# Kernel tuning notes

Measured on AMD Instinct MI355X. Metric: run time of the kernel, lower is better.

## Reference

```python
import jax, jax.numpy as jnp
import numpy as np

B, L, D_IN, D_MODEL, N_LAYERS, D_STATE, D_OUT = 32, 1024, 3, 512, 4, 64, 10


def setup_inputs() -> dict:
    key = jax.random.key(0)
    ks = jax.random.split(key, 6)
    x = jax.random.normal(ks[0], (B, L, D_IN), jnp.float32)
    W_enc = jax.random.normal(ks[1], (D_IN, D_MODEL), jnp.float32) / np.sqrt(D_IN)
    # per-channel log timestep, standard S4 init range [1e-3, 1e-1]
    log_dt = jax.random.uniform(ks[2], (N_LAYERS, D_MODEL), jnp.float32,
                                minval=np.log(1e-3), maxval=np.log(1e-1))
    # S4D-real init: A_n = -(n + 1/2), stored as log of magnitude
    A_log = jnp.broadcast_to(
        jnp.log(0.5 + jnp.arange(D_STATE, dtype=jnp.float32)),
        (N_LAYERS, D_MODEL, D_STATE)) * jnp.ones((), jnp.float32)
    C = jax.random.normal(ks[3], (N_LAYERS, D_MODEL, D_STATE), jnp.float32) / np.sqrt(D_STATE)
    W_ff = jax.random.normal(ks[4], (N_LAYERS, D_MODEL, D_MODEL), jnp.float32) / np.sqrt(D_MODEL)
    W_dec = jax.random.normal(ks[5], (D_MODEL, D_OUT), jnp.float32) / np.sqrt(D_MODEL)
    return dict(x=x, W_enc=W_enc, log_dt=log_dt, A_log=A_log, C=C, W_ff=W_ff, W_dec=W_dec)


def _s4d(x, log_dt, A_log, C):
    """Diagonal real S4D layer (is_real=True, skip=False, identity activation).
    x: (B, L, H); log_dt: (H,); A_log, C: (H, N).
    """
    Lx = x.shape[1]
    dt = jnp.exp(log_dt)                         # (H,)
    A = -jnp.exp(A_log)                          # (H, N) real negative poles
    dtA = dt[:, None] * A                        # (H, N)
    Bbar = (jnp.exp(dtA) - 1.0) / A              # ZOH discretization with B = 1
    # Vandermonde kernel: K[h, l] = sum_n (C*Bbar)[h, n] * exp(dtA[h, n] * l)
    lrange = jnp.arange(Lx, dtype=x.dtype)
    K = jnp.einsum('hn,hnl->hl', C * Bbar, jnp.exp(dtA[:, :, None] * lrange))
    # causal depthwise convolution via FFT (linear conv, pad to 2L)
    n = 2 * Lx
    Kf = jnp.fft.rfft(K, n=n, axis=-1)           # (H, n//2+1)
    xf = jnp.fft.rfft(x, n=n, axis=1)            # (B, n//2+1, H)
    y = jnp.fft.irfft(xf * Kf.T[None], n=n, axis=1)[:, :Lx]
    return y


def reference(x, W_enc, log_dt, A_log, C, W_ff, W_dec):
    h = x @ W_enc                                # (B, L, d_model), bias=False
    for i in range(N_LAYERS):
        h = _s4d(h, log_dt[i], A_log[i], C[i])   # S4D layer
        # dropout is identity at inference; FF block: Linear(no bias) + ReLU
        h = jax.nn.relu(h @ W_ff[i])
    out = h @ W_dec                              # (B, L, d_output)
    return out[:, -1, :]                         # get_last=True -> (B, d_output)
```

## Files before the change

### kernel.cpp

```cpp
#include <hip/hip_runtime.h>
#include <math.h>

#define B_   32
#define L_   1024
#define BT_  (B_*L_)
#define DIN  3
#define H_   512
#define NL   4
#define NS   64
#define DOUT 10
#define CT   128
#define NC   (L_/CT)
#define BH   (B_*H_)

typedef __attribute__((ext_vector_type(8))) _Float16 f16x8;
typedef __attribute__((ext_vector_type(4))) float f32x4;

__device__ inline void gload16(const void* g, void* l) {
    __builtin_amdgcn_global_load_lds((const __attribute__((address_space(1))) void*)g,
                                     (__attribute__((address_space(3))) void*)l, 16, 0, 0);
}

#define PSW(row, col) ((row) * 64 + ((col) ^ (((row) & 7) << 3)))

#define RAW_BARRIER() do { \
    asm volatile("s_waitcnt lgkmcnt(0)" ::: "memory"); \
    __builtin_amdgcn_s_barrier(); \
    asm volatile("" ::: "memory"); } while (0)

__global__ __launch_bounds__(512, 4) void conv_fused(const float* __restrict__ x,
                                                     const float* __restrict__ Wenc,
                                                     const float* __restrict__ log_dt,
                                                     const float* __restrict__ A_log,
                                                     const float* __restrict__ Cmat,
                                                     const float* __restrict__ WffL,
                                                     _Float16* __restrict__ WTl,
                                                     const _Float16* __restrict__ XT,
                                                     _Float16* __restrict__ YT,
                                                     float* __restrict__ ylast,
                                                     int layer, int doY) {
    __shared__ __align__(16) _Float16 smem[32768];
    __shared__ float Kl4[4][128];
    __shared__ float Kl[128];
    __shared__ float dAs[64];
    __shared__ float wps[64];
    __shared__ float rTs[64];
    _Float16* Vl  = smem;
    _Float16* Xh0 = smem + 8192;
    _Float16* Pl  = smem + 16384;
    _Float16* X1r = smem + 24576;
    _Float16* S0l = smem + 24576;
    _Float16* Bp  = smem;

    int bid = blockIdx.x;
    int h = bid >> 1, mh = bid & 1;
    int tid = threadIdx.x;
    int w = tid >> 6, l = tid & 63;
    const int fr = l & 15, q = l >> 4;
    const int wm = w >> 1, wn = w & 1;
    const _Float16* Xh = XT + (size_t)h * BT_ + (size_t)mh * 16384;

    const int c = l & 7, rsub = l >> 3;
    float w0e = 0.f, w1e = 0.f, w2e = 0.f;
    if (layer == 0) { w0e = Wenc[h]; w1e = Wenc[H_ + h]; w2e = Wenc[2 * H_ + h]; }

    if (layer == 0) {
#pragma unroll
        for (int s = 0; s < 2; s++) {
            _Float16* dst = s ? X1r : Xh0;
#pragma unroll
            for (int ii = 0; ii < 2; ii++) {
                int t2 = w * 2 + ii;
                int rr = t2 * 8 + rsub;
                int srcc = c ^ (rr & 7);
                int bt = mh * 16384 + rr * 128 + s * 64 + srcc * 8;
                const float* xp = x + (size_t)bt * DIN;
                f16x8 o;
#pragma unroll
                for (int e = 0; e < 8; e++)
                    o[e] = (_Float16)fmaf(xp[e * 3], w0e,
                                     fmaf(xp[e * 3 + 1], w1e, xp[e * 3 + 2] * w2e));
                *(f16x8*)&dst[t2 * 512 + l * 8] = o;
            }
        }
    } else {
#pragma unroll
        for (int s = 0; s < 2; s++) {
            _Float16* dst = s ? X1r : Xh0;
#pragma unroll
            for (int ii = 0; ii < 2; ii++) {
                int t2 = w * 2 + ii;
                int rr = t2 * 8 + rsub;
                int srcc = c ^ (rr & 7);
                gload16(Xh + (size_t)rr * 128 + s * 64 + srcc * 8,
                        &dst[t2 * 512 + l * 8]);
            }
        }
    }

    if (tid < 64) {
        int n = tid;
        float dt  = expf(log_dt[layer * H_ + h]);
        float A   = -expf(A_log[((size_t)layer * H_ + h) * NS + n]);
        float dtA = dt * A;
        float r0  = expf(dtA);
        dAs[n] = dtA;
        wps[n] = Cmat[((size_t)layer * H_ + h) * NS + n] * ((r0 - 1.0f) / A);
        rTs[n] = expf(dtA * (float)CT);
    } else if (layer < 3 && tid < 96) {
        int g = bid * 32 + (tid - 64);
        int n = g >> 6, k8 = g & 63;
        const float* src = WffL + n;
        f16x8 o;
#pragma unroll
        for (int j = 0; j < 8; j++)
            o[j] = (_Float16)src[(size_t)(k8 * 8 + j) * H_];
        *(f16x8*)(WTl + (size_t)n * H_ + k8 * 8) = o;
    }
    RAW_BARRIER();

#pragma unroll
    for (int ii = 0; ii < 2; ii++) {
        int slot = tid + 512 * ii;
        int n = slot >> 4, cc = slot & 15;
        float da = dAs[n];
        int jb = cc * 8;
        float cur  = __expf(da * (float)(127 - jb));
        float rinv = __expf(-da);
        f16x8 vv;
#pragma unroll
        for (int e = 0; e < 8; e++) { vv[e] = (_Float16)cur; cur *= rinv; }
        *(f16x8*)&Vl[n * 128 + ((cc >> 3) * 8 + ((cc & 7) ^ (n & 7))) * 8] = vv;
    }
    if (doY) {
        int t = tid & 127, g = tid >> 7;
        float k = 0.f, d = (float)t;
        for (int n = g * 16; n < g * 16 + 16; n++) k += wps[n] * __expf(dAs[n] * d);
        Kl4[g][t] = k;
    }
    __syncthreads();

    if (doY && tid < 128)
        Kl[tid] = (Kl4[0][tid] + Kl4[1][tid]) + (Kl4[2][tid] + Kl4[3][tid]);

    f16x8 fA[2][2][2];
    f32x4 accP[2][2] = {};
#pragma unroll
    for (int i = 0; i < 2; i++)
#pragma unroll
        for (int kk = 0; kk < 2; kk++) {
            int row = wm * 32 + i * 16 + fr;
            int kc = kk * 4 + q;
            fA[i][0][kk] = *(const f16x8*)&Xh0[row * 64 + ((kc ^ (row & 7)) * 8)];
            fA[i][1][kk] = *(const f16x8*)&X1r[row * 64 + ((kc ^ (row & 7)) * 8)];
        }
#pragma unroll
    for (int s = 0; s < 2; s++)
#pragma unroll
        for (int kk = 0; kk < 2; kk++) {
            int kc = kk * 4 + q;
            f16x8 bv[2];
#pragma unroll
            for (int j = 0; j < 2; j++) {
                int n = wn * 32 + j * 16 + fr;
                bv[j] = *(const f16x8*)&Vl[n * 128 + s * 64 + ((kc ^ (n & 7)) * 8)];
            }
#pragma unroll
            for (int i = 0; i < 2; i++)
#pragma unroll
                for (int j = 0; j < 2; j++)
                    accP[i][j] = __builtin_amdgcn_mfma_f32_16x16x32_f16(
                        fA[i][s][kk], bv[j], accP[i][j], 0, 0, 0);
        }

#pragma unroll
    for (int i = 0; i < 2; i++)
#pragma unroll
        for (int j = 0; j < 2; j++)
#pragma unroll
            for (int tt = 0; tt < 4; tt++) {
                int row = wm * 32 + i * 16 + q * 4 + tt;
                int col = wn * 32 + j * 16 + fr;
                Pl[PSW(row, col)] = (_Float16)accP[i][j][tt];
            }
    __syncthreads();

#pragma unroll
    for (int ii = 0; ii < 2; ii++) {
        int slot = tid + 512 * ii;
        int bl = slot >> 6, n = slot & 63;
        float rTn = rTs[n];
        float E = 0.f;
        if (doY) {
#pragma unroll
            for (int cc = 0; cc < 8; cc++) {
                int row = bl * 8 + cc;
                S0l[row * 64 + (((n >> 3) ^ (row & 7)) * 8 + (n & 7))] = (_Float16)E;
                E = fmaf(rTn, E, (float)Pl[PSW(row, n)]);
            }
        } else {
#pragma unroll
            for (int cc = 0; cc < 8; cc++) {
                int row = bl * 8 + cc;
                E = fmaf(rTn, E, (float)Pl[PSW(row, n)]);
            }
            float wE = wps[n] * E;
            wE += __shfl_xor(wE, 32); wE += __shfl_xor(wE, 16);
            wE += __shfl_xor(wE, 8);  wE += __shfl_xor(wE, 4);
            wE += __shfl_xor(wE, 2);  wE += __shfl_xor(wE, 1);
            if (l == 0) ylast[(size_t)(mh * 16 + bl) * H_ + h] = wE;
        }
    }
    if (!doY) return;
    __syncthreads();

#pragma unroll
    for (int ii = 0; ii < 2; ii++) {
        int slot = tid + 512 * ii;
        int n = slot & 63, tc = slot >> 6;
        int t0 = tc * 8;
        float ratio = __expf(dAs[n]);
        float cur   = wps[n] * __expf(dAs[n] * (float)(t0 + 1));
#pragma unroll
        for (int e = 0; e < 8; e++) {
            Bp[(t0 + e) * 192 + (16 + ((n >> 3) ^ e)) * 8 + (n & 7)] = (_Float16)cur;
            cur *= ratio;
        }
    }
#pragma unroll
    for (int ii = 0; ii < 4; ii++) {
        int slot = tid + 512 * ii;
        int t = slot >> 4, cc = slot & 15;
        _Float16* bp = &Bp[t * 192 + ((cc >> 3) * 8 + ((cc & 7) ^ (t & 7))) * 8];
        int jb = cc * 8;
#pragma unroll
        for (int e = 0; e < 8; e++) {
            int j = jb + e;
            bp[e] = (j <= t) ? (_Float16)Kl[t - j] : (_Float16)0.f;
        }
    }
    __syncthreads();

    f32x4 acc[2][4] = {};
#pragma unroll
    for (int s = 0; s < 3; s++)
#pragma unroll
        for (int kk = 0; kk < 2; kk++) {
            int kc = kk * 4 + q;
            f16x8 av[2], bv[4];
#pragma unroll
            for (int i = 0; i < 2; i++) {
                int row = wm * 32 + i * 16 + fr;
                av[i] = (s < 2) ? fA[i][s][kk]
                                : *(const f16x8*)&S0l[row * 64 + ((kc ^ (row & 7)) * 8)];
            }
#pragma unroll
            for (int j = 0; j < 4; j++) {
                int tc = wn * 64 + j * 16 + fr;
                bv[j] = *(const f16x8*)&Bp[tc * 192 + (s * 8 + (kc ^ (tc & 7))) * 8];
            }
#pragma unroll
            for (int i = 0; i < 2; i++)
#pragma unroll
                for (int j = 0; j < 4; j++)
                    acc[i][j] = __builtin_amdgcn_mfma_f32_16x16x32_f16(av[i], bv[j], acc[i][j], 0, 0, 0);
        }

    __syncthreads();
#pragma unroll
    for (int i = 0; i < 2; i++)
#pragma unroll
        for (int j = 0; j < 4; j++)
#pragma unroll
            for (int tt = 0; tt < 4; tt++) {
                int row = wm * 32 + i * 16 + q * 4 + tt;
                int col = wn * 64 + j * 16 + fr;
                smem[row * 136 + col] = (_Float16)acc[i][j][tt];
            }
    __syncthreads();
    _Float16* Yp = YT + (size_t)h * BT_ + (size_t)mh * 16384;
#pragma unroll
    for (int k2 = 0; k2 < 4; k2++) {
        int ch = tid + 512 * k2;
        int r = ch >> 4, c8 = ch & 15;
        *(f16x8*)(Yp + (size_t)r * 128 + c8 * 8) = *(const f16x8*)&smem[r * 136 + c8 * 8];
    }
}

__global__ __launch_bounds__(256) void ffn_gemm_T(
    const _Float16* __restrict__ WT,
    const _Float16* __restrict__ YT,
    _Float16* __restrict__ OT)
{
    __shared__ __align__(16) _Float16 pool[20736];
    _Float16* As0 = pool;
    _Float16* Bs0 = pool + 12288;
    const int tid = threadIdx.x;
    const int l = tid & 63, w = tid >> 6;
    const int bt0 = blockIdx.x * 128;
    const int bn  = blockIdx.y * 128;
    const int srow = l >> 2, schunk = (l & 3) ^ ((l >> 3) & 3);
    const _Float16* ga0 = WT + (size_t)(bn + (w * 2 + 0) * 16 + srow) * H_ + schunk * 8;
    const _Float16* ga1 = WT + (size_t)(bn + (w * 2 + 1) * 16 + srow) * H_ + schunk * 8;
    const int btg = tid & 15, kp = tid >> 4;
    const _Float16* gb = YT + (size_t)(kp * 2) * BT_ + bt0 + btg * 8;

    f16x8 stB[2][2];
    f32x4 acc[4][4] = {};

    auto loadB = [&](int ks, int st) {
        stB[st][0] = *(const f16x8*)(gb + (size_t)(ks * 32) * BT_);
        stB[st][1] = *(const f16x8*)(gb + (size_t)(ks * 32 + 1) * BT_);
    };
    auto stageA = [&](int ks, int buf) {
        gload16(ga0 + ks * 32, As0 + buf * 4096 + (w * 2 + 0) * 512);
        gload16(ga1 + ks * 32, As0 + buf * 4096 + (w * 2 + 1) * 512);
    };
    auto writeB = [&](int st, int buf) {
        const int kpc = kp >> 2, kps = kp & 3;
#pragma unroll
        for (int e = 0; e < 8; e++) {
            int row = btg * 8 + e;
            int off = row * 32 + (row >> 3) * 8 + ((kpc ^ ((row >> 1) & 3)) * 8) + kps * 2;
            _Float16 lo = stB[st][0][e], hi = stB[st][1][e];
            unsigned v = (unsigned)__builtin_bit_cast(unsigned short, lo)
                       | ((unsigned)__builtin_bit_cast(unsigned short, hi) << 16);
            *(unsigned*)&Bs0[buf * 4224 + off] = v;
        }
    };

    loadB(0, 0);
    loadB(1, 1);
    __builtin_amdgcn_sched_barrier(0);
    stageA(0, 0);
    stageA(1, 1);
    writeB(0, 0);
    asm volatile("s_waitcnt vmcnt(2) lgkmcnt(0)" ::: "memory");
    __builtin_amdgcn_s_barrier();
    asm volatile("" ::: "memory");

    const int wm = w >> 1, wn = w & 1;
    const int fr = l & 15, q = l >> 4;
    const int axor = ((fr >> 1) & 3);
#pragma unroll
    for (int ks = 0; ks < 16; ks++) {
        const int a_cur = ks % 3;
        const int b_cur = ks & 1;
        if (ks + 2 < 16) {
            loadB(ks + 2, b_cur);
            __builtin_amdgcn_sched_barrier(0);
            stageA(ks + 2, (ks + 2) % 3);
        }
        f16x8 av[4], bv[4];
#pragma unroll
        for (int i = 0; i < 4; i++) {
            int row = wm * 64 + i * 16 + fr;
            av[i] = *(const f16x8*)&As0[a_cur * 4096 + row * 32 + ((q ^ axor) * 8)];
        }
#pragma unroll
        for (int j = 0; j < 4; j++) {
            int row = wn * 64 + j * 16 + fr;
            bv[j] = *(const f16x8*)&Bs0[b_cur * 4224 + row * 32 + (row >> 3) * 8
                                        + ((q ^ ((row >> 1) & 3)) * 8)];
        }
#pragma unroll
        for (int i = 0; i < 4; i++)
#pragma unroll
            for (int j = 0; j < 4; j++)
                acc[i][j] = __builtin_amdgcn_mfma_f32_16x16x32_f16(av[i], bv[j], acc[i][j], 0, 0, 0);
        if (ks + 1 < 16) {
            writeB((ks + 1) & 1, b_cur ^ 1);
            if (ks + 2 < 16)
                asm volatile("s_waitcnt vmcnt(4) lgkmcnt(0)" ::: "memory");
            else
                asm volatile("s_waitcnt vmcnt(0) lgkmcnt(0)" ::: "memory");
            __builtin_amdgcn_s_barrier();
            asm volatile("" ::: "memory");
        }
    }
    asm volatile("s_waitcnt lgkmcnt(0)" ::: "memory");
    __builtin_amdgcn_s_barrier();
    asm volatile("" ::: "memory");

#pragma unroll
    for (int half = 0; half < 2; half++) {
        if (half) __syncthreads();
        if (wm == half) {
#pragma unroll
            for (int i = 0; i < 4; i++)
#pragma unroll
                for (int j = 0; j < 4; j++)
#pragma unroll
                    for (int tt = 0; tt < 4; tt++) {
                        int r  = i * 16 + q * 4 + tt;
                        int cc = wn * 64 + j * 16 + fr;
                        pool[r * 136 + cc] = (_Float16)fmaxf(acc[i][j][tt], 0.f);
                    }
        }
        __syncthreads();
#pragma unroll
        for (int k2 = 0; k2 < 4; k2++) {
            int ch = tid + 256 * k2;
            int r = ch >> 4, c8 = ch & 15;
            *(f16x8*)(OT + (size_t)(bn + half * 64 + r) * BT_ + bt0 + c8 * 8) =
                *(const f16x8*)&pool[r * 136 + c8 * 8];
        }
    }
}

__global__ __launch_bounds__(512) void final_head(const float* __restrict__ ylast,
                                                  const float* __restrict__ Wff3,
                                                  const float* __restrict__ Wdec,
                                                  float* __restrict__ out) {
    int b = blockIdx.x;
    int t = threadIdx.x;
    __shared__ float yrow[H_];
    __shared__ float hrow[H_];
    yrow[t] = ylast[(size_t)b * H_ + t];
    __syncthreads();
    float acc = 0.f;
    for (int k = 0; k < H_; k++) acc = fmaf(yrow[k], Wff3[(size_t)k * H_ + t], acc);
    hrow[t] = fmaxf(acc, 0.f);
    __syncthreads();
    if (t < DOUT) {
        float o = 0.f;
        for (int k = 0; k < H_; k++) o = fmaf(hrow[k], Wdec[(size_t)k * DOUT + t], o);
        out[(size_t)b * DOUT + t] = o;
    }
}

extern "C" void kernel_launch(void* const* d_in, const int* in_sizes, int n_in,
                              void* d_out, int out_size, void* d_ws, size_t ws_size,
                              hipStream_t stream) {
    const float* x      = (const float*)d_in[0];
    const float* Wenc   = (const float*)d_in[1];
    const float* log_dt = (const float*)d_in[2];
    const float* A_log  = (const float*)d_in[3];
    const float* Cmat   = (const float*)d_in[4];
    const float* Wff    = (const float*)d_in[5];
    const float* Wdec   = (const float*)d_in[6];
    float* out = (float*)d_out;

    char* ws = (char*)d_ws;
    _Float16* bufA  = (_Float16*)(ws);
    _Float16* bufB  = (_Float16*)(ws + 33554432);
    _Float16* WT    = (_Float16*)(ws + 68681728);
    float*    ylast = (float*)(ws + 70254592);

    for (int l = 0; l < NL; l++) {
        if (l < NL - 1) {
            conv_fused<<<H_ * 2, 512, 0, stream>>>(x, Wenc, log_dt, A_log, Cmat,
                                                   Wff + (size_t)l * H_ * H_,
                                                   WT + (size_t)l * H_ * H_,
                                                   bufA, bufB, ylast, l, 1);
            ffn_gemm_T<<<dim3(BT_ / 128, H_ / 128), 256, 0, stream>>>(
                WT + (size_t)l * H_ * H_, bufB, bufA);
        } else {
            conv_fused<<<H_ * 2, 512, 0, stream>>>(x, Wenc, log_dt, A_log, Cmat,
                                                   Wff + (size_t)l * H_ * H_,
                                                   WT,
                                                   bufA, bufB, ylast, l, 0);
            final_head<<<B_, 512, 0, stream>>>(ylast, Wff + (size_t)l * H_ * H_, Wdec, out);
        }
    }
}
```

Baseline: 211.3 us.

## Widen FFN GEMM tile to 256 columns and parallelize final head

The FFN GEMM block grows from 256 to 512 threads, and each block now covers 256 batch-time columns instead of 128. The 128-row weight tile is shared across twice as many columns and each thread stages one A chunk instead of two, with the wait counts and LDS strides adjusted to match. The final head is split into 8 blocks per batch row: each computes a 64-column slice with split-K partial sums and atomically adds its decoder contribution into an output that conv layer 0 zeroes. The costs are more LDS per GEMM block, fewer GEMM blocks, and float atomics in the head, which make the summation order nondeterministic.

```diff
diff --git a/kernel.cpp b/kernel.cpp
--- a/kernel.cpp
+++ b/kernel.cpp
@@ -38,6 +38,7 @@
                                                      const _Float16* __restrict__ XT,
                                                      _Float16* __restrict__ YT,
                                                      float* __restrict__ ylast,
+                                                     float* __restrict__ outz,
                                                      int layer, int doY) {
     __shared__ __align__(16) _Float16 smem[32768];
     __shared__ float Kl4[4][128];
@@ -65,6 +66,7 @@
     if (layer == 0) { w0e = Wenc[h]; w1e = Wenc[H_ + h]; w2e = Wenc[2 * H_ + h]; }
 
     if (layer == 0) {
+        if (bid == 0 && tid < B_ * DOUT) outz[tid] = 0.f;
 #pragma unroll
         for (int s = 0; s < 2; s++) {
             _Float16* dst = s ? X1r : Xh0;
@@ -287,23 +289,22 @@
     }
 }
 
-__global__ __launch_bounds__(256) void ffn_gemm_T(
+__global__ __launch_bounds__(512, 4) void ffn_gemm_T(
     const _Float16* __restrict__ WT,
     const _Float16* __restrict__ YT,
     _Float16* __restrict__ OT)
 {
-    __shared__ __align__(16) _Float16 pool[20736];
+    __shared__ __align__(16) _Float16 pool[29184];
     _Float16* As0 = pool;
     _Float16* Bs0 = pool + 12288;
     const int tid = threadIdx.x;
     const int l = tid & 63, w = tid >> 6;
-    const int bt0 = blockIdx.x * 128;
+    const int bt0 = blockIdx.x * 256;
     const int bn  = blockIdx.y * 128;
     const int srow = l >> 2, schunk = (l & 3) ^ ((l >> 3) & 3);
-    const _Float16* ga0 = WT + (size_t)(bn + (w * 2 + 0) * 16 + srow) * H_ + schunk * 8;
-    const _Float16* ga1 = WT + (size_t)(bn + (w * 2 + 1) * 16 + srow) * H_ + schunk * 8;
-    const int btg = tid & 15, kp = tid >> 4;
-    const _Float16* gb = YT + (size_t)(kp * 2) * BT_ + bt0 + btg * 8;
+    const _Float16* ga0 = WT + (size_t)(bn + w * 16 + srow) * H_ + schunk * 8;
+    const int btg = tid & 15, kp = (tid >> 4) & 15, bth = tid >> 8;
+    const _Float16* gb = YT + (size_t)(kp * 2) * BT_ + bt0 + bth * 128 + btg * 8;
 
     f16x8 stB[2][2];
     f32x4 acc[4][4] = {};
@@ -313,19 +314,18 @@
         stB[st][1] = *(const f16x8*)(gb + (size_t)(ks * 32 + 1) * BT_);
     };
     auto stageA = [&](int ks, int buf) {
-        gload16(ga0 + ks * 32, As0 + buf * 4096 + (w * 2 + 0) * 512);
-        gload16(ga1 + ks * 32, As0 + buf * 4096 + (w * 2 + 1) * 512);
+        gload16(ga0 + ks * 32, As0 + buf * 4096 + w * 512);
     };
     auto writeB = [&](int st, int buf) {
         const int kpc = kp >> 2, kps = kp & 3;
 #pragma unroll
         for (int e = 0; e < 8; e++) {
-            int row = btg * 8 + e;
+            int row = bth * 128 + btg * 8 + e;
             int off = row * 32 + (row >> 3) * 8 + ((kpc ^ ((row >> 1) & 3)) * 8) + kps * 2;
             _Float16 lo = stB[st][0][e], hi = stB[st][1][e];
             unsigned v = (unsigned)__builtin_bit_cast(unsigned short, lo)
                        | ((unsigned)__builtin_bit_cast(unsigned short, hi) << 16);
-            *(unsigned*)&Bs0[buf * 4224 + off] = v;
+            *(unsigned*)&Bs0[buf * 8448 + off] = v;
         }
     };
 
@@ -335,11 +335,11 @@
     stageA(0, 0);
     stageA(1, 1);
     writeB(0, 0);
-    asm volatile("s_waitcnt vmcnt(2) lgkmcnt(0)" ::: "memory");
+    asm volatile("s_waitcnt vmcnt(1) lgkmcnt(0)" ::: "memory");
     __builtin_amdgcn_s_barrier();
     asm volatile("" ::: "memory");
 
-    const int wm = w >> 1, wn = w & 1;
+    const int wm = w >> 2, wn = w & 3;
     const int fr = l & 15, q = l >> 4;
     const int axor = ((fr >> 1) & 3);
 #pragma unroll
@@ -360,7 +360,7 @@
 #pragma unroll
         for (int j = 0; j < 4; j++) {
             int row = wn * 64 + j * 16 + fr;
-            bv[j] = *(const f16x8*)&Bs0[b_cur * 4224 + row * 32 + (row >> 3) * 8
+            bv[j] = *(const f16x8*)&Bs0[b_cur * 8448 + row * 32 + (row >> 3) * 8
                                         + ((q ^ ((row >> 1) & 3)) * 8)];
         }
 #pragma unroll
@@ -371,7 +371,7 @@
         if (ks + 1 < 16) {
             writeB((ks + 1) & 1, b_cur ^ 1);
             if (ks + 2 < 16)
-                asm volatile("s_waitcnt vmcnt(4) lgkmcnt(0)" ::: "memory");
+                asm volatile("s_waitcnt vmcnt(3) lgkmcnt(0)" ::: "memory");
             else
                 asm volatile("s_waitcnt vmcnt(0) lgkmcnt(0)" ::: "memory");
             __builtin_amdgcn_s_barrier();
@@ -394,38 +394,52 @@
                     for (int tt = 0; tt < 4; tt++) {
                         int r  = i * 16 + q * 4 + tt;
                         int cc = wn * 64 + j * 16 + fr;
-                        pool[r * 136 + cc] = (_Float16)fmaxf(acc[i][j][tt], 0.f);
+                        pool[r * 264 + cc] = (_Float16)fmaxf(acc[i][j][tt], 0.f);
                     }
         }
         __syncthreads();
 #pragma unroll
         for (int k2 = 0; k2 < 4; k2++) {
-            int ch = tid + 256 * k2;
-            int r = ch >> 4, c8 = ch & 15;
+            int ch = tid + 512 * k2;
+            int r = ch >> 5, c8 = ch & 31;
             *(f16x8*)(OT + (size_t)(bn + half * 64 + r) * BT_ + bt0 + c8 * 8) =
-                *(const f16x8*)&pool[r * 136 + c8 * 8];
+                *(const f16x8*)&pool[r * 264 + c8 * 8];
         }
     }
 }
 
-__global__ __launch_bounds__(512) void final_head(const float* __restrict__ ylast,
-                                                  const float* __restrict__ Wff3,
-                                                  const float* __restrict__ Wdec,
-                                                  float* __restrict__ out) {
-    int b = blockIdx.x;
-    int t = threadIdx.x;
+__global__ __launch_bounds__(512) void final_head2(const float* __restrict__ ylast,
+                                                   const float* __restrict__ Wff3,
+                                                   const float* __restrict__ Wdec,
+                                                   float* __restrict__ out) {
+    int bid = blockIdx.x;
+    int b = bid >> 3, s = bid & 7;
+    int tid = threadIdx.x;
     __shared__ float yrow[H_];
-    __shared__ float hrow[H_];
-    yrow[t] = ylast[(size_t)b * H_ + t];
-    __syncthreads();
+    __shared__ float hpart[8][64];
+    yrow[tid] = ylast[(size_t)b * H_ + tid];
+    __syncthreads();
+    int kg = tid >> 6, tl = tid & 63;
+    int t = s * 64 + tl;
     float acc = 0.f;
-    for (int k = 0; k < H_; k++) acc = fmaf(yrow[k], Wff3[(size_t)k * H_ + t], acc);
-    hrow[t] = fmaxf(acc, 0.f);
-    __syncthreads();
-    if (t < DOUT) {
-        float o = 0.f;
-        for (int k = 0; k < H_; k++) o = fmaf(hrow[k], Wdec[(size_t)k * DOUT + t], o);
-        out[(size_t)b * DOUT + t] = o;
+    const float* wcol = Wff3 + t;
+    for (int k = kg * 64; k < kg * 64 + 64; k++)
+        acc = fmaf(yrow[k], wcol[(size_t)k * H_], acc);
+    hpart[kg][tl] = acc;
+    __syncthreads();
+    if (tid < 64) {
+        float hv = 0.f;
+#pragma unroll
+        for (int g = 0; g < 8; g++) hv += hpart[g][tid];
+        hv = fmaxf(hv, 0.f);
+#pragma unroll
+        for (int d = 0; d < DOUT; d++) {
+            float v = hv * Wdec[(size_t)(s * 64 + tid) * DOUT + d];
+            v += __shfl_xor(v, 32); v += __shfl_xor(v, 16);
+            v += __shfl_xor(v, 8);  v += __shfl_xor(v, 4);
+            v += __shfl_xor(v, 2);  v += __shfl_xor(v, 1);
+            if (tid == 0) atomicAdd(&out[(size_t)b * DOUT + d], v);
+        }
     }
 }
 
@@ -452,15 +466,15 @@
             conv_fused<<<H_ * 2, 512, 0, stream>>>(x, Wenc, log_dt, A_log, Cmat,
                                                    Wff + (size_t)l * H_ * H_,
                                                    WT + (size_t)l * H_ * H_,
-                                                   bufA, bufB, ylast, l, 1);
-            ffn_gemm_T<<<dim3(BT_ / 128, H_ / 128), 256, 0, stream>>>(
+                                                   bufA, bufB, ylast, out, l, 1);
+            ffn_gemm_T<<<dim3(BT_ / 256, H_ / 128), 512, 0, stream>>>(
                 WT + (size_t)l * H_ * H_, bufB, bufA);
         } else {
             conv_fused<<<H_ * 2, 512, 0, stream>>>(x, Wenc, log_dt, A_log, Cmat,
                                                    Wff + (size_t)l * H_ * H_,
                                                    WT,
-                                                   bufA, bufB, ylast, l, 0);
-            final_head<<<B_, 512, 0, stream>>>(ylast, Wff + (size_t)l * H_ * H_, Wdec, out);
+                                                   bufA, bufB, ylast, out, l, 0);
+            final_head2<<<B_ * 8, 512, 0, stream>>>(ylast, Wff + (size_t)l * H_ * H_, Wdec, out);
         }
     }
 }
```

New measurement: 188.7 us. 10.7% less time.
